# Kernel optimization log

Hardware: AMD Instinct MI355X
Metric: run time of the kernel (lower is better)

Reference implementation:

```python
import jax, jax.numpy as jnp
import numpy as np

N_NODES = 100000
N_EDGES = 1600000
IN_CH = 128
HID = 128   # 2 * out_channels
OUT_CH = 64


def setup_inputs() -> dict:
    key = jax.random.key(0)
    k1, k2, k3, k4, k5, k6 = jax.random.split(key, 6)
    x = jax.random.normal(k1, (N_NODES, IN_CH), dtype=jnp.float32)
    edge_index = jax.random.randint(k2, (2, N_EDGES), 0, N_NODES, dtype=jnp.int64)
    W1 = jax.random.normal(k3, (IN_CH, HID), dtype=jnp.float32) / np.sqrt(IN_CH)
    b1 = jax.random.normal(k4, (HID,), dtype=jnp.float32) * 0.01
    W2 = jax.random.normal(k5, (HID, OUT_CH), dtype=jnp.float32) / np.sqrt(HID)
    b2 = jax.random.normal(k6, (OUT_CH,), dtype=jnp.float32) * 0.01
    return {"x": x, "edge_index": edge_index, "W1": W1, "b1": b1, "W2": W2, "b2": b2}


def _gcn_layer(x, src, dst, norm, W, b, n_nodes):
    # GCNConv: linear transform, then normalized scatter-add aggregation + bias
    h = x @ W                                   # [N, d_out]
    msg = h[src] * norm[:, None]                # gather + edge normalize, [E+N, d_out]
    out = jax.ops.segment_sum(msg, dst, num_segments=n_nodes)
    return out + b


def reference(x, edge_index, W1, b1, W2, b2):
    n = x.shape[0]
    loop = jnp.arange(n, dtype=edge_index.dtype)
    # add self-loops (PyG GCNConv default)
    src = jnp.concatenate([edge_index[0], loop])
    dst = jnp.concatenate([edge_index[1], loop])
    # symmetric normalization deg^-1/2[src] * deg^-1/2[dst]
    deg = jax.ops.segment_sum(jnp.ones_like(dst, x.dtype), dst, num_segments=n)
    dinv = jnp.where(deg > 0, jax.lax.rsqrt(deg), 0.0)
    norm = dinv[src] * dinv[dst]

    h = jax.nn.relu(_gcn_layer(x, src, dst, norm, W1, b1, n))
    out = jax.nn.relu(_gcn_layer(h, src, dst, norm, W2, b2, n))
    return out
```

## Files before the change

### kernel.cpp

```cpp
#include <hip/hip_runtime.h>
#include <hip/hip_fp16.h>
#include <math.h>

typedef _Float16 f16x8 __attribute__((ext_vector_type(8)));
typedef float f32x4 __attribute__((ext_vector_type(4)));

#define BSH 8
#define BSZ 256

__global__ __launch_bounds__(256) void passA(const int* __restrict__ ei,
                                             int* __restrict__ bcount, int E, int NB) {
  __shared__ int hist[512];
  int t = threadIdx.x;
  hist[t] = 0;
  hist[t + 256] = 0;
  __syncthreads();
  for (int e = blockIdx.x * 256 + t; e < E; e += gridDim.x * 256)
    atomicAdd(&hist[ei[E + e] >> BSH], 1);
  __syncthreads();
  if (t < NB && hist[t]) atomicAdd(&bcount[t], hist[t]);
  int t2 = t + 256;
  if (t2 < NB && hist[t2]) atomicAdd(&bcount[t2], hist[t2]);
}

__global__ __launch_bounds__(512) void scanB(const int* __restrict__ bcount,
                                             int* __restrict__ bstart,
                                             int* __restrict__ bfill, int NB, int E) {
  __shared__ int s[512];
  int t = threadIdx.x;
  int v = (t < NB) ? bcount[t] : 0;
  s[t] = v;
  __syncthreads();
  for (int off = 1; off < 512; off <<= 1) {
    int add = (t >= off) ? s[t - off] : 0;
    __syncthreads();
    s[t] += add;
    __syncthreads();
  }
  if (t < NB) {
    int ex = s[t] - v;
    bstart[t] = ex;
    bfill[t] = ex;
  }
  if (t == 0) bstart[NB] = E;
}

template <int NC, int NWC, bool IN_F16, bool SCALE>
__device__ __forceinline__ void gemm_mfma_body(
    const void* __restrict__ Xv, const float* __restrict__ W,
    const float* __restrict__ dinv, _Float16* __restrict__ G, int nrows, int bid,
    _Float16* Bs) {
  int t = threadIdx.x;
  {
    int n = t % NC;
    int kh = (t / NC) * (NC / 2);
    constexpr int NBLK = (NC / 2) / 8;
#pragma unroll
    for (int b = 0; b < NBLK; ++b) {
      f16x8 tmp;
#pragma unroll
      for (int j = 0; j < 8; ++j)
        tmp[j] = (_Float16)W[(size_t)(kh + b * 8 + j) * NC + n];
      *(f16x8*)(&Bs[n * 136 + kh + b * 8]) = tmp;
    }
  }
  __syncthreads();

  int w = t >> 6, lane = t & 63;
  int m = lane & 15, q = lane >> 4;
  int wr = (w / NWC) * 64, wc = (w % NWC) * 64;
  constexpr int ROWS = (4 / NWC) * 64;
  int row0 = bid * ROWS;

  auto loadA = [&](int kc, f16x8* dst) {
    int kbase = kc * 32 + q * 8;
#pragma unroll
    for (int rt = 0; rt < 4; ++rt) {
      int row = row0 + wr + rt * 16 + m;
      if constexpr (IN_F16) {
        f16x8 a = {0, 0, 0, 0, 0, 0, 0, 0};
        if (row < nrows)
          a = *(const f16x8*)((const _Float16*)Xv + (size_t)row * NC * (128 / NC) +
                              kbase);
        dst[rt] = a;
      } else {
        float4 x0 = {0, 0, 0, 0}, x1 = {0, 0, 0, 0};
        if (row < nrows) {
          const float* Xf = (const float*)Xv;
          x0 = *(const float4*)(Xf + (size_t)row * 128 + kbase);
          x1 = *(const float4*)(Xf + (size_t)row * 128 + kbase + 4);
        }
        f16x8 a;
        a[0] = (_Float16)x0.x; a[1] = (_Float16)x0.y;
        a[2] = (_Float16)x0.z; a[3] = (_Float16)x0.w;
        a[4] = (_Float16)x1.x; a[5] = (_Float16)x1.y;
        a[6] = (_Float16)x1.z; a[7] = (_Float16)x1.w;
        dst[rt] = a;
      }
    }
  };

  f32x4 acc[4][4];
#pragma unroll
  for (int rt = 0; rt < 4; ++rt)
#pragma unroll
    for (int ct = 0; ct < 4; ++ct)
#pragma unroll
      for (int qq = 0; qq < 4; ++qq) acc[rt][ct][qq] = 0.f;

  f16x8 af[4];
  loadA(0, af);
#pragma unroll
  for (int kc = 0; kc < 4; ++kc) {
    f16x8 afn[4];
    if (kc < 3) loadA(kc + 1, afn);
    int kbase = kc * 32 + q * 8;
    f16x8 bf[4];
#pragma unroll
    for (int ct = 0; ct < 4; ++ct) {
      int n = wc + ct * 16 + m;
      bf[ct] = *(f16x8*)(&Bs[n * 136 + kbase]);
    }
#pragma unroll
    for (int rt = 0; rt < 4; ++rt)
#pragma unroll
      for (int ct = 0; ct < 4; ++ct)
        acc[rt][ct] = __builtin_amdgcn_mfma_f32_16x16x32_f16(af[rt], bf[ct],
                                                             acc[rt][ct], 0, 0, 0);
    if (kc < 3) {
#pragma unroll
      for (int rt = 0; rt < 4; ++rt) af[rt] = afn[rt];
    }
  }

  __syncthreads();
  _Float16* Ct = Bs;
  constexpr int CPITCH = NC + 8;
#pragma unroll
  for (int rt = 0; rt < 4; ++rt) {
#pragma unroll
    for (int r = 0; r < 4; ++r) {
      int lrow = wr + rt * 16 + q * 4 + r;
      int grow = row0 + lrow;
      float d = 1.f;
      if (SCALE) d = (grow < nrows) ? dinv[grow] : 1.f;
#pragma unroll
      for (int ct = 0; ct < 4; ++ct)
        Ct[lrow * CPITCH + wc + ct * 16 + m] = (_Float16)(acc[rt][ct][r] * d);
    }
  }
  __syncthreads();
  constexpr int C8 = NC / 8;
  for (int idx = t; idx < ROWS * C8; idx += 256) {
    int lrow = idx / C8, c8 = (idx % C8) * 8;
    int grow = row0 + lrow;
    if (grow < nrows)
      *(f16x8*)(G + (size_t)grow * NC + c8) = *(const f16x8*)(Ct + lrow * CPITCH + c8);
  }
}

__global__ __launch_bounds__(256) void fused_gemm_passB(
    const float* __restrict__ X, const float* __restrict__ W1,
    _Float16* __restrict__ G, int nrows, int GB,
    const int* __restrict__ ei, int* __restrict__ bfill,
    unsigned int* __restrict__ pairs, int E, int PB) {
  __shared__ char smem[128 * 136 * 2];
  int g = blockIdx.x;
  int M2 = 2 * (GB < PB ? GB : PB);
  bool is_gemm;
  int bid;
  if (g < M2) { is_gemm = (g & 1) == 0; bid = g >> 1; }
  else        { is_gemm = (GB > PB);    bid = g - M2 + (GB < PB ? GB : PB); }
  if (is_gemm) {
    gemm_mfma_body<128, 2, false, false>(X, W1, nullptr, G, nrows, bid,
                                         (_Float16*)smem);
  } else {
    int* hist = (int*)smem;
    int* gbase = (int*)(smem + 2048);
    int t = threadIdx.x;
    hist[t] = 0;
    hist[t + 256] = 0;
    __syncthreads();
    int d[8], s[8], lp[8], bb[8];
    int base = bid * 2048;
#pragma unroll
    for (int u = 0; u < 8; ++u) {
      int e = base + u * 256 + t;
      if (e < E) {
        d[u] = ei[E + e];
        s[u] = ei[e];
        bb[u] = d[u] >> BSH;
        lp[u] = atomicAdd(&hist[bb[u]], 1);
      } else {
        bb[u] = -1;
      }
    }
    __syncthreads();
    if (hist[t]) gbase[t] = atomicAdd(&bfill[t], hist[t]);
    int t2 = t + 256;
    if (hist[t2]) gbase[t2] = atomicAdd(&bfill[t2], hist[t2]);
    __syncthreads();
#pragma unroll
    for (int u = 0; u < 8; ++u)
      if (bb[u] >= 0)
        pairs[gbase[bb[u]] + lp[u]] =
            ((unsigned int)(d[u] & (BSZ - 1)) << 17) | (unsigned int)s[u];
  }
}

__global__ __launch_bounds__(256) void gemm2_mfma(const _Float16* __restrict__ X,
                                                  const float* __restrict__ W,
                                                  const float* __restrict__ dinv,
                                                  _Float16* __restrict__ G, int nrows) {
  __shared__ char smem2[256 * 72 * 2];
  gemm_mfma_body<64, 1, true, true>(X, W, dinv, G, nrows, blockIdx.x,
                                    (_Float16*)smem2);
}

__global__ __launch_bounds__(512) void passC(const unsigned int* __restrict__ pairs,
                                             const int* __restrict__ bstart,
                                             int* __restrict__ rowstart,
                                             int* __restrict__ deg,
                                             float* __restrict__ dinv,
                                             int* __restrict__ csr, int N) {
  __shared__ int hcnt[BSZ];
  __shared__ int lfill[BSZ];
  __shared__ int ss[BSZ];
  int b = blockIdx.x;
  int t = threadIdx.x;
  int lo = bstart[b], hi = bstart[b + 1];
  int nbase = b << BSH;
  if (t < BSZ) hcnt[t] = 0;
  __syncthreads();
  for (int k = lo + t; k < hi; k += 512)
    atomicAdd(&hcnt[(pairs[k] >> 17) & (BSZ - 1)], 1);
  __syncthreads();
  int v = 0;
  if (t < BSZ) {
    v = hcnt[t];
    ss[t] = v;
  }
  __syncthreads();
  for (int off = 1; off < BSZ; off <<= 1) {
    int add = (t < BSZ && t >= off) ? ss[t - off] : 0;
    __syncthreads();
    if (t < BSZ) ss[t] += add;
    __syncthreads();
  }
  if (t < BSZ) {
    int ex = ss[t] - v;
    lfill[t] = ex;
    int node = nbase + t;
    if (node < N) {
      rowstart[node] = lo + ex;
      deg[node] = v;
      dinv[node] = rsqrtf((float)v + 1.f);
    }
  }
  __syncthreads();
  for (int k = lo + t; k < hi; k += 512) {
    unsigned int p = pairs[k];
    int pos = atomicAdd(&lfill[(p >> 17) & (BSZ - 1)], 1);
    csr[lo + pos] = (int)(p & 0x1FFFFu);
  }
}

__global__ __launch_bounds__(256) void agg128(
    const __half* __restrict__ G, const int* __restrict__ csr,
    const int* __restrict__ rowstart, const int* __restrict__ deg,
    const float* __restrict__ dinv, const float* __restrict__ bias,
    __half* __restrict__ out, int n) {
  int wid = blockIdx.x * 4 + (threadIdx.x >> 6);
  if (wid >= n) return;
  int i = __builtin_amdgcn_readfirstlane(wid);
  int lane = threadIdx.x & 63;
  int g = lane >> 4;
  int c = lane & 15;
  const _Float16* Gh = (const _Float16*)G;
  float di = dinv[i];
  f16x8 self = *(const f16x8*)(Gh + (size_t)i * 128 + c * 8);
  float wself = (g == 0) ? di : 0.f;
  float a[8];
#pragma unroll
  for (int j = 0; j < 8; ++j) a[j] = wself * (float)self[j];
  int s = rowstart[i];
  int d = deg[i];
  for (int base = 0; base < d; base += 64) {
    int chunk = d - base;
    if (chunk > 64) chunk = 64;
    int myidx = (lane < chunk) ? csr[s + base + lane] : i;
    for (int k = 0; k < chunk; k += 8) {
      int sl0 = k + g, sl1 = k + 4 + g;
      int s0 = __shfl(myidx, sl0);
      int s1 = __shfl(myidx, sl1);
      float w0 = dinv[s0];
      float w1 = dinv[s1];
      if (sl0 >= chunk) w0 = 0.f;
      if (sl1 >= chunk) w1 = 0.f;
      f16x8 v0 = *(const f16x8*)(Gh + (size_t)s0 * 128 + c * 8);
      f16x8 v1 = *(const f16x8*)(Gh + (size_t)s1 * 128 + c * 8);
#pragma unroll
      for (int j = 0; j < 8; ++j) a[j] = fmaf(w0, (float)v0[j], a[j]);
#pragma unroll
      for (int j = 0; j < 8; ++j) a[j] = fmaf(w1, (float)v1[j], a[j]);
    }
  }
#pragma unroll
  for (int j = 0; j < 8; ++j) {
    a[j] += __shfl_xor(a[j], 16);
    a[j] += __shfl_xor(a[j], 32);
  }
  if (g == 0) {
    float4 b0 = *(const float4*)(bias + c * 8);
    float4 b1 = *(const float4*)(bias + c * 8 + 4);
    f16x8 r;
    r[0] = (_Float16)fmaxf(fmaf(di, a[0], b0.x), 0.f);
    r[1] = (_Float16)fmaxf(fmaf(di, a[1], b0.y), 0.f);
    r[2] = (_Float16)fmaxf(fmaf(di, a[2], b0.z), 0.f);
    r[3] = (_Float16)fmaxf(fmaf(di, a[3], b0.w), 0.f);
    r[4] = (_Float16)fmaxf(fmaf(di, a[4], b1.x), 0.f);
    r[5] = (_Float16)fmaxf(fmaf(di, a[5], b1.y), 0.f);
    r[6] = (_Float16)fmaxf(fmaf(di, a[6], b1.z), 0.f);
    r[7] = (_Float16)fmaxf(fmaf(di, a[7], b1.w), 0.f);
    *(f16x8*)((_Float16*)out + (size_t)i * 128 + c * 8) = r;
  }
}

__global__ __launch_bounds__(256) void agg64(
    const __half* __restrict__ G, const int* __restrict__ csr,
    const int* __restrict__ rowstart, const int* __restrict__ deg,
    const float* __restrict__ dinv, const float* __restrict__ bias,
    float* __restrict__ out, int n) {
  typedef _Float16 f16x4 __attribute__((ext_vector_type(4)));
  int wid = blockIdx.x * 4 + (threadIdx.x >> 6);
  if (wid >= n) return;
  int i = __builtin_amdgcn_readfirstlane(wid);
  int lane = threadIdx.x & 63;
  int g = lane >> 4;
  int c = lane & 15;
  const _Float16* Gh = (const _Float16*)G;
  f16x4 self = *(const f16x4*)(Gh + (size_t)i * 64 + c * 4);
  float wself = (g == 0) ? 1.f : 0.f;
  float a[4];
#pragma unroll
  for (int j = 0; j < 4; ++j) a[j] = wself * (float)self[j];
  int s = rowstart[i];
  int d = deg[i];
  for (int base = 0; base < d; base += 64) {
    int chunk = d - base;
    if (chunk > 64) chunk = 64;
    int myidx = (lane < chunk) ? csr[s + base + lane] : i;
    for (int k = 0; k < chunk; k += 8) {
      int sl0 = k + g, sl1 = k + 4 + g;
      int s0 = __shfl(myidx, sl0);
      int s1 = __shfl(myidx, sl1);
      float w0 = (sl0 < chunk) ? 1.f : 0.f;
      float w1 = (sl1 < chunk) ? 1.f : 0.f;
      f16x4 v0 = *(const f16x4*)(Gh + (size_t)s0 * 64 + c * 4);
      f16x4 v1 = *(const f16x4*)(Gh + (size_t)s1 * 64 + c * 4);
#pragma unroll
      for (int j = 0; j < 4; ++j) a[j] = fmaf(w0, (float)v0[j], a[j]);
#pragma unroll
      for (int j = 0; j < 4; ++j) a[j] = fmaf(w1, (float)v1[j], a[j]);
    }
  }
#pragma unroll
  for (int j = 0; j < 4; ++j) {
    a[j] += __shfl_xor(a[j], 16);
    a[j] += __shfl_xor(a[j], 32);
  }
  if (g == 0) {
    float di = dinv[i];
    float4 bv = *(const float4*)(bias + c * 4);
    float4 r;
    r.x = fmaxf(fmaf(di, a[0], bv.x), 0.f);
    r.y = fmaxf(fmaf(di, a[1], bv.y), 0.f);
    r.z = fmaxf(fmaf(di, a[2], bv.z), 0.f);
    r.w = fmaxf(fmaf(di, a[3], bv.w), 0.f);
    *(float4*)(out + (size_t)i * 64 + c * 4) = r;
  }
}

extern "C" void kernel_launch(void* const* d_in, const int* in_sizes, int n_in,
                              void* d_out, int out_size, void* d_ws, size_t ws_size,
                              hipStream_t stream) {
  const float* x  = (const float*)d_in[0];
  const int*   ei = (const int*)d_in[1];
  const float* W1 = (const float*)d_in[2];
  const float* b1 = (const float*)d_in[3];
  const float* W2 = (const float*)d_in[4];
  const float* b2 = (const float*)d_in[5];
  float* out = (float*)d_out;

  const int N = in_sizes[0] / 128;
  const int E = in_sizes[1] / 2;
  const int NB = (N + BSZ - 1) >> BSH;

  char* base = (char*)d_ws;
  size_t off = 0;
  auto alloc = [&](size_t bytes) -> void* {
    void* p = base + off;
    off += (bytes + 255) & ~(size_t)255;
    return p;
  };
  int*          bcount   = (int*)alloc(512 * 4);
  int*          bstart   = (int*)alloc(516 * 4);
  int*          bfill    = (int*)alloc(512 * 4);
  int*          deg      = (int*)alloc((size_t)N * 4);
  int*          rowstart = (int*)alloc((size_t)N * 4);
  float*        dinv     = (float*)alloc((size_t)N * 4);
  int*          csr      = (int*)alloc((size_t)E * 4 + 256);
  unsigned int* pairs    = (unsigned int*)alloc((size_t)E * 4);
  __half*       g1       = (__half*)alloc((size_t)N * 128 * 2);
  __half*       x2       = (__half*)alloc((size_t)N * 128 * 2);

  hipMemsetAsync(bcount, 0, 512 * 4, stream);
  passA<<<512, 256, 0, stream>>>(ei, bcount, E, NB);
  scanB<<<1, 512, 0, stream>>>(bcount, bstart, bfill, NB, E);

  int GB = (N + 127) / 128;
  int PB = (E + 2047) / 2048;
  fused_gemm_passB<<<GB + PB, 256, 0, stream>>>(x, W1, (_Float16*)g1, N, GB, ei,
                                                bfill, pairs, E, PB);
  passC<<<NB, 512, 0, stream>>>(pairs, bstart, rowstart, deg, dinv, csr, N);

  agg128<<<(N + 3) / 4, 256, 0, stream>>>(g1, csr, rowstart, deg, dinv, b1, x2, N);
  int G2B = (N + 255) / 256;
  gemm2_mfma<<<G2B, 256, 0, stream>>>((const _Float16*)x2, W2, dinv,
                                      (_Float16*)g1, N);
  agg64<<<(N + 3) / 4, 256, 0, stream>>>(g1, csr, rowstart, deg, dinv, b2, out, N);
}
```

Baseline: 291.6 us.

## Load GEMM weight fragments directly into registers and drop LDS staging

```diff
diff --git a/kernel.cpp b/kernel.cpp
--- a/kernel.cpp
+++ b/kernel.cpp
@@ -45,31 +45,17 @@
   if (t == 0) bstart[NB] = E;
 }
 
-template <int NC, int NWC, bool IN_F16, bool SCALE>
-__device__ __forceinline__ void gemm_mfma_body(
+template <int NC, bool IN_F16, bool SCALE>
+__device__ __forceinline__ void gemm_reg_body(
     const void* __restrict__ Xv, const float* __restrict__ W,
-    const float* __restrict__ dinv, _Float16* __restrict__ G, int nrows, int bid,
-    _Float16* Bs) {
+    const float* __restrict__ dinv, _Float16* __restrict__ G,
+    int nrows, int bid) {
   int t = threadIdx.x;
-  {
-    int n = t % NC;
-    int kh = (t / NC) * (NC / 2);
-    constexpr int NBLK = (NC / 2) / 8;
-#pragma unroll
-    for (int b = 0; b < NBLK; ++b) {
-      f16x8 tmp;
-#pragma unroll
-      for (int j = 0; j < 8; ++j)
-        tmp[j] = (_Float16)W[(size_t)(kh + b * 8 + j) * NC + n];
-      *(f16x8*)(&Bs[n * 136 + kh + b * 8]) = tmp;
-    }
-  }
-  __syncthreads();
-
   int w = t >> 6, lane = t & 63;
   int m = lane & 15, q = lane >> 4;
+  constexpr int NWC = NC / 64;
+  constexpr int ROWS = (4 / NWC) * 64;
   int wr = (w / NWC) * 64, wc = (w % NWC) * 64;
-  constexpr int ROWS = (4 / NWC) * 64;
   int row0 = bid * ROWS;
 
   auto loadA = [&](int kc, f16x8* dst) {
@@ -80,8 +66,7 @@
       if constexpr (IN_F16) {
         f16x8 a = {0, 0, 0, 0, 0, 0, 0, 0};
         if (row < nrows)
-          a = *(const f16x8*)((const _Float16*)Xv + (size_t)row * NC * (128 / NC) +
-                              kbase);
+          a = *(const f16x8*)((const _Float16*)Xv + (size_t)row * 128 + kbase);
         dst[rt] = a;
       } else {
         float4 x0 = {0, 0, 0, 0}, x1 = {0, 0, 0, 0};
@@ -100,32 +85,41 @@
     }
   };
 
-  f32x4 acc[4][4];
-#pragma unroll
-  for (int rt = 0; rt < 4; ++rt)
-#pragma unroll
-    for (int ct = 0; ct < 4; ++ct)
-#pragma unroll
-      for (int qq = 0; qq < 4; ++qq) acc[rt][ct][qq] = 0.f;
-
   f16x8 af[4];
   loadA(0, af);
+
+  f16x8 bf[4][4];
+#pragma unroll
+  for (int kc = 0; kc < 4; ++kc) {
+    int kbase = kc * 32 + q * 8;
+#pragma unroll
+    for (int ct = 0; ct < 4; ++ct) {
+      int n = wc + ct * 16 + m;
+      f16x8 bb;
+#pragma unroll
+      for (int j = 0; j < 8; ++j)
+        bb[j] = (_Float16)W[(size_t)(kbase + j) * NC + n];
+      bf[kc][ct] = bb;
+    }
+  }
+
+  f32x4 acc[4][4];
+#pragma unroll
+  for (int rt = 0; rt < 4; ++rt)
+#pragma unroll
+    for (int ct = 0; ct < 4; ++ct)
+#pragma unroll
+      for (int qq = 0; qq < 4; ++qq) acc[rt][ct][qq] = 0.f;
+
 #pragma unroll
   for (int kc = 0; kc < 4; ++kc) {
     f16x8 afn[4];
     if (kc < 3) loadA(kc + 1, afn);
-    int kbase = kc * 32 + q * 8;
-    f16x8 bf[4];
-#pragma unroll
-    for (int ct = 0; ct < 4; ++ct) {
-      int n = wc + ct * 16 + m;
-      bf[ct] = *(f16x8*)(&Bs[n * 136 + kbase]);
-    }
 #pragma unroll
     for (int rt = 0; rt < 4; ++rt)
 #pragma unroll
       for (int ct = 0; ct < 4; ++ct)
-        acc[rt][ct] = __builtin_amdgcn_mfma_f32_16x16x32_f16(af[rt], bf[ct],
+        acc[rt][ct] = __builtin_amdgcn_mfma_f32_16x16x32_f16(af[rt], bf[kc][ct],
                                                              acc[rt][ct], 0, 0, 0);
     if (kc < 3) {
 #pragma unroll
@@ -133,29 +127,18 @@
     }
   }
 
-  __syncthreads();
-  _Float16* Ct = Bs;
-  constexpr int CPITCH = NC + 8;
 #pragma unroll
   for (int rt = 0; rt < 4; ++rt) {
 #pragma unroll
     for (int r = 0; r < 4; ++r) {
-      int lrow = wr + rt * 16 + q * 4 + r;
-      int grow = row0 + lrow;
-      float d = 1.f;
-      if (SCALE) d = (grow < nrows) ? dinv[grow] : 1.f;
-#pragma unroll
-      for (int ct = 0; ct < 4; ++ct)
-        Ct[lrow * CPITCH + wc + ct * 16 + m] = (_Float16)(acc[rt][ct][r] * d);
-    }
-  }
-  __syncthreads();
-  constexpr int C8 = NC / 8;
-  for (int idx = t; idx < ROWS * C8; idx += 256) {
-    int lrow = idx / C8, c8 = (idx % C8) * 8;
-    int grow = row0 + lrow;
-    if (grow < nrows)
-      *(f16x8*)(G + (size_t)grow * NC + c8) = *(const f16x8*)(Ct + lrow * CPITCH + c8);
+      int row = row0 + wr + rt * 16 + q * 4 + r;
+      if (row < nrows) {
+        float d = SCALE ? dinv[row] : 1.f;
+#pragma unroll
+        for (int ct = 0; ct < 4; ++ct)
+          G[(size_t)row * NC + wc + ct * 16 + m] = (_Float16)(acc[rt][ct][r] * d);
+      }
+    }
   }
 }
 
@@ -164,7 +147,7 @@
     _Float16* __restrict__ G, int nrows, int GB,
     const int* __restrict__ ei, int* __restrict__ bfill,
     unsigned int* __restrict__ pairs, int E, int PB) {
-  __shared__ char smem[128 * 136 * 2];
+  __shared__ int smem[1024];
   int g = blockIdx.x;
   int M2 = 2 * (GB < PB ? GB : PB);
   bool is_gemm;
@@ -172,11 +155,10 @@
   if (g < M2) { is_gemm = (g & 1) == 0; bid = g >> 1; }
   else        { is_gemm = (GB > PB);    bid = g - M2 + (GB < PB ? GB : PB); }
   if (is_gemm) {
-    gemm_mfma_body<128, 2, false, false>(X, W1, nullptr, G, nrows, bid,
-                                         (_Float16*)smem);
+    gemm_reg_body<128, false, false>(X, W1, nullptr, G, nrows, bid);
   } else {
-    int* hist = (int*)smem;
-    int* gbase = (int*)(smem + 2048);
+    int* hist = smem;
+    int* gbase = smem + 512;
     int t = threadIdx.x;
     hist[t] = 0;
     hist[t + 256] = 0;
@@ -212,9 +194,7 @@
                                                   const float* __restrict__ W,
                                                   const float* __restrict__ dinv,
                                                   _Float16* __restrict__ G, int nrows) {
-  __shared__ char smem2[256 * 72 * 2];
-  gemm_mfma_body<64, 1, true, true>(X, W, dinv, G, nrows, blockIdx.x,
-                                    (_Float16*)smem2);
+  gemm_reg_body<64, true, true>(X, W, dinv, G, nrows, blockIdx.x);
 }
 
 __global__ __launch_bounds__(512) void passC(const unsigned int* __restrict__ pairs,
```

Measured after the change: 315.2 us. 1.08x slower.
